# Kernel optimization log

Hardware: AMD Instinct MI355X
Metric: run time of the kernel (lower is better)

Reference implementation:

```python
import jax, jax.numpy as jnp
import numpy as np

TOP_K = 2  # config.num_active_experts


def setup_inputs() -> dict:
    key = jax.random.key(0)
    k1, k2, k3, k4 = jax.random.split(key, 4)
    B, S, D = 2, 2048, 1024
    E, W = 8, 1024  # 8 experts, each width 1024 -> total_expert_width = 8192
    x = jax.random.normal(k1, (B, S, D), dtype=jnp.float32)
    router_w = jax.random.normal(k2, (E, D), dtype=jnp.float32) * 0.02
    w1 = jax.random.normal(k3, (D, E * W), dtype=jnp.float32) * 0.02
    w2 = jax.random.normal(k4, (E * W, D), dtype=jnp.float32) * 0.02
    return {"x": x, "router_w": router_w, "w1": w1, "w2": w2}


def reference(x, router_w, w1, w2):
    B, S, D = x.shape
    E = router_w.shape[0]
    W = w1.shape[1] // E  # uniform expert width
    T = B * S
    xf = x.reshape(T, D)

    # Router: sigmoid gating, top-k, sum-normalized weights (norm_topk_prob)
    router_logits = jnp.einsum('td,ed->te', xf, router_w)
    router_probs = jax.nn.sigmoid(router_logits.astype(jnp.float32))
    top_w, sel = jax.lax.top_k(router_probs, TOP_K)          # [T,K]
    top_w = top_w / (top_w.sum(axis=-1, keepdims=True) + 1e-20)
    top_w = top_w.astype(x.dtype)

    # Expert MLPs: expert e uses w1[:, off_e:off_e+W], w2[off_e:off_e+W, :].
    # Uniform width -> single batched einsum over experts (same math as the
    # padded-gather / block-sparse SDD/DSD grouped GEMM pipeline).
    W1e = w1.reshape(D, E, W).transpose(1, 0, 2)             # [E,D,W]
    W2e = w2.reshape(E, W, D)                                # [E,W,D]
    h = jnp.einsum('td,edw->etw', xf, W1e)                   # up-proj
    a = jnp.square(jax.nn.relu(h))                           # relu_squared
    y = jnp.einsum('etw,ewd->etd', a, W2e)                   # down-proj

    # Weighted scatter-combine: combine_weights[t,e] = top_w if e selected else 0
    cw = jnp.zeros((T, E), dtype=x.dtype).at[jnp.arange(T)[:, None], sel].set(top_w)
    out = jnp.einsum('etd,te->td', y, cw)
    return out.reshape(B, S, D)
```

## Files before the change

### kernel.cpp

```cpp
#include <hip/hip_runtime.h>
#include <hip/hip_bf16.h>


#define T_TOKENS 4096
#define DD 1024
#define EE 8
#define WW 1024
#define CAP 1536
#define BM 128
#define BN 128
#define BK 64
#define MT (CAP / BM)
#define NT (WW / BN)
#define GEMM_BLOCKS (EE * MT * NT)
#define TR1_BLOCKS 2048
#define TR2_BLOCKS 2048

typedef short bf16x8 __attribute__((ext_vector_type(8)));
typedef float f32x4 __attribute__((ext_vector_type(4)));

__device__ __forceinline__ void gload_lds16(const void* g, void* l) {
  __builtin_amdgcn_global_load_lds((__attribute__((address_space(1))) void*)(g),
                                   (__attribute__((address_space(3))) void*)(l),
                                   16, 0, 0);
}

__device__ __forceinline__ float bf2f(unsigned short u) {
  union { unsigned int i; float f; } v; v.i = (unsigned int)u << 16; return v.f;
}

__global__ __launch_bounds__(256) void pre_kernel(
    const float* __restrict__ w1, const float* __restrict__ x,
    const float* __restrict__ rw,
    __hip_bfloat16* __restrict__ w1t, __hip_bfloat16* __restrict__ xb,
    int* __restrict__ sel, float* __restrict__ wpair)
{
  __shared__ float tile[64][65];
  int b = blockIdx.x;
  if (b < TR1_BLOCKS) {
    int bx = b & 15;
    int by = b >> 4;
    const float* src = w1;
    __hip_bfloat16* dst = w1t;
    long src_ld = EE * WW, dst_ld = DD;
    long c0 = (long)bx * 64;
    long r0 = (long)by * 64;
    int tx = threadIdx.x & 15, ty = threadIdx.x >> 4;
#pragma unroll
    for (int i = 0; i < 4; i++) {
      int sr = ty + 16 * i;
      f32x4 v = *(const f32x4*)(src + (c0 + sr) * src_ld + r0 + tx * 4);
      tile[sr][tx * 4 + 0] = v[0];
      tile[sr][tx * 4 + 1] = v[1];
      tile[sr][tx * 4 + 2] = v[2];
      tile[sr][tx * 4 + 3] = v[3];
    }
    __syncthreads();
#pragma unroll
    for (int i = 0; i < 4; i++) {
      int dr = ty + 16 * i;
      union { __hip_bfloat16 hb[4]; ushort4 u4; } pk;
#pragma unroll
      for (int j = 0; j < 4; j++)
        pk.hb[j] = __float2bfloat16(tile[tx * 4 + j][dr]);
      *(ushort4*)((unsigned short*)dst + (r0 + dr) * dst_ld + c0 + tx * 4) = pk.u4;
    }
  } else {
    int lane = threadIdx.x & 63;
    int wave = threadIdx.x >> 6;
    int t = (b - TR1_BLOCKS) * 4 + wave;
    const float* xrow = x + (size_t)t * DD;
    float acc[EE];
#pragma unroll
    for (int e = 0; e < EE; e++) acc[e] = 0.f;
#pragma unroll
    for (int i = 0; i < DD / 64; i++) {
      int d = lane + i * 64;
      float xv = xrow[d];
      xb[t * DD + d] = __float2bfloat16(xv);
#pragma unroll
      for (int e = 0; e < EE; e++) acc[e] += xv * rw[e * DD + d];
    }
#pragma unroll
    for (int e = 0; e < EE; e++) {
#pragma unroll
      for (int off = 32; off > 0; off >>= 1)
        acc[e] += __shfl_down(acc[e], off, 64);
    }
    if (lane == 0) {
      float p[EE];
#pragma unroll
      for (int e = 0; e < EE; e++) p[e] = 1.f / (1.f + expf(-acc[e]));
      int e0 = 0; float b0 = p[0];
      for (int e = 1; e < EE; e++) if (p[e] > b0) { b0 = p[e]; e0 = e; }
      int e1 = -1; float b1 = -1.f;
      for (int e = 0; e < EE; e++) {
        if (e == e0) continue;
        if (p[e] > b1) { b1 = p[e]; e1 = e; }
      }
      float s = b0 + b1 + 1e-20f;
      sel[t] = e0 | (e1 << 8);
      wpair[2 * t]     = b0 / s;
      wpair[2 * t + 1] = b1 / s;
    }
  }
}

__global__ __launch_bounds__(1024) void build_lists(
    const int* __restrict__ sel, int* __restrict__ counts,
    int* __restrict__ idx, int* __restrict__ tslot)
{
  __shared__ int lcnt[EE];
  int tid = threadIdx.x, lane = tid & 63;
  if (tid < EE) lcnt[tid] = 0;
  __syncthreads();
  unsigned long long lower = (1ull << lane) - 1;
#pragma unroll
  for (int j = 0; j < T_TOKENS / 1024; j++) {
    int t = j * 1024 + tid;
    int s = sel[t];
    int e0 = s & 0xff, e1 = (s >> 8) & 0xff;
    int slot0 = 0, slot1 = 0;
#pragma unroll
    for (int e = 0; e < EE; e++) {
      unsigned long long m0 = __ballot(e0 == e);
      unsigned long long m1 = __ballot(e1 == e);
      int c0 = __popcll(m0), c1 = __popcll(m1);
      int base = 0;
      if (lane == 0 && (c0 + c1) > 0) base = atomicAdd(&lcnt[e], c0 + c1);
      base = __shfl(base, 0, 64);
      if (e0 == e) slot0 = base + __popcll(m0 & lower);
      if (e1 == e) slot1 = base + c0 + __popcll(m1 & lower);
    }
    int p0 = e0 * CAP + slot0, p1 = e1 * CAP + slot1;
    idx[p0] = t; idx[p1] = t;
    tslot[2 * t] = p0; tslot[2 * t + 1] = p1;
  }
  __syncthreads();
  if (tid < EE) counts[tid] = lcnt[tid];
}

__global__ __launch_bounds__(256, 3) void gemm1_kernel(
    const __hip_bfloat16* __restrict__ xb, const __hip_bfloat16* __restrict__ w1t,
    const int* __restrict__ counts, const int* __restrict__ idx,
    __hip_bfloat16* __restrict__ act,
    const float* __restrict__ w2, __hip_bfloat16* __restrict__ w2t)
{
  __shared__ __attribute__((aligned(16))) char smem[32768];
  int bid = blockIdx.x;
  if (bid >= GEMM_BLOCKS) {
    float (*tile)[65] = (float (*)[65])smem;
    int b2 = bid - GEMM_BLOCKS;
    int bx = b2 & 15;
    int z = b2 >> 4;
    int e = z >> 4, yy = z & 15;
    const float* src = w2 + (long)e * WW * DD;
    __hip_bfloat16* dst = w2t + (long)e * DD * WW;
    long src_ld = DD, dst_ld = WW;
    long c0 = (long)bx * 64;
    long r0 = (long)yy * 64;
    int tx = threadIdx.x & 15, ty = threadIdx.x >> 4;
#pragma unroll
    for (int i = 0; i < 4; i++) {
      int sr = ty + 16 * i;
      f32x4 v = *(const f32x4*)(src + (c0 + sr) * src_ld + r0 + tx * 4);
      tile[sr][tx * 4 + 0] = v[0];
      tile[sr][tx * 4 + 1] = v[1];
      tile[sr][tx * 4 + 2] = v[2];
      tile[sr][tx * 4 + 3] = v[3];
    }
    __syncthreads();
#pragma unroll
    for (int i = 0; i < 4; i++) {
      int dr = ty + 16 * i;
      union { __hip_bfloat16 hb[4]; ushort4 u4; } pk;
#pragma unroll
      for (int j = 0; j < 4; j++)
        pk.hb[j] = __float2bfloat16(tile[tx * 4 + j][dr]);
      *(ushort4*)((unsigned short*)dst + (r0 + dr) * dst_ld + c0 + tx * 4) = pk.u4;
    }
    return;
  }
  short* As = (short*)smem;
  short* Bs = (short*)(smem + 16384);
  int e = bid & 7;
  int i = bid >> 3;
  int mt = i >> 3, nt = i & 7;
  int n_e = counts[e];
  if (mt * BM >= n_e) return;

  int tid = threadIdx.x;
  int lane = tid & 63;
  int wave = __builtin_amdgcn_readfirstlane(tid >> 6);
  int wm = (wave >> 1) * 64, wn = (wave & 1) * 64;
  int m16 = lane & 15, qd = lane >> 4;

  const __hip_bfloat16* gA[4];
  const __hip_bfloat16* gB[4];
#pragma unroll
  for (int i2 = 0; i2 < 4; i2++) {
    int s = i2 * 256 + tid;
    int r = s >> 3;
    int q = (s & 7) ^ (r & 7);
    int rowA = mt * BM + r;
    int slot = rowA < n_e ? rowA : n_e - 1;
    int tok = idx[e * CAP + slot];
    gA[i2] = xb + (size_t)tok * DD + q * 8;
    gB[i2] = w1t + ((size_t)e * WW + nt * BN + r) * DD + q * 8;
  }
  short* ldsA[4];
  short* ldsB[4];
#pragma unroll
  for (int i2 = 0; i2 < 4; i2++) {
    ldsA[i2] = As + (i2 * 256 + wave * 64) * 8;
    ldsB[i2] = Bs + (i2 * 256 + wave * 64) * 8;
  }

  int aoff[4][2], boff[4][2];
#pragma unroll
  for (int mi = 0; mi < 4; mi++) {
    int r = wm + mi * 16 + m16;
#pragma unroll
    for (int h = 0; h < 2; h++)
      aoff[mi][h] = (r * 8 + ((qd + h * 4) ^ (r & 7))) * 8;
  }
#pragma unroll
  for (int ni = 0; ni < 4; ni++) {
    int r = wn + ni * 16 + m16;
#pragma unroll
    for (int h = 0; h < 2; h++)
      boff[ni][h] = (r * 8 + ((qd + h * 4) ^ (r & 7))) * 8;
  }

  f32x4 zero = {0.f, 0.f, 0.f, 0.f};
  f32x4 acc[4][4];
#pragma unroll
  for (int mi = 0; mi < 4; mi++)
#pragma unroll
    for (int ni = 0; ni < 4; ni++) acc[mi][ni] = zero;

  for (int k0 = 0; k0 < DD; k0 += BK) {
#pragma unroll
    for (int i2 = 0; i2 < 4; i2++) gload_lds16(gA[i2] + k0, ldsA[i2]);
#pragma unroll
    for (int i2 = 0; i2 < 4; i2++) gload_lds16(gB[i2] + k0, ldsB[i2]);
    __syncthreads();
#pragma unroll
    for (int h = 0; h < 2; h++) {
      bf16x8 af[4], bfr[4];
#pragma unroll
      for (int mi = 0; mi < 4; mi++) af[mi] = *(const bf16x8*)(As + aoff[mi][h]);
#pragma unroll
      for (int ni = 0; ni < 4; ni++) bfr[ni] = *(const bf16x8*)(Bs + boff[ni][h]);
#pragma unroll
      for (int mi = 0; mi < 4; mi++)
#pragma unroll
        for (int ni = 0; ni < 4; ni++)
          acc[mi][ni] = __builtin_amdgcn_mfma_f32_16x16x32_bf16(
              af[mi], bfr[ni], acc[mi][ni], 0, 0, 0);
    }
    __syncthreads();
  }

#pragma unroll
  for (int mi = 0; mi < 4; mi++) {
#pragma unroll
    for (int reg = 0; reg < 4; reg++) {
      int rowt = mt * BM + wm + mi * 16 + qd * 4 + reg;
      if (rowt < n_e) {
#pragma unroll
        for (int ni = 0; ni < 4; ni++) {
          float v = acc[mi][ni][reg];
          v = v > 0.f ? v * v : 0.f;
          int col = nt * BN + wn + ni * 16 + m16;
          act[((size_t)e * CAP + rowt) * WW + col] = __float2bfloat16(v);
        }
      }
    }
  }
}

__global__ __launch_bounds__(256, 3) void gemm2_kernel(
    const __hip_bfloat16* __restrict__ act, const __hip_bfloat16* __restrict__ w2t,
    const int* __restrict__ counts, __hip_bfloat16* __restrict__ y)
{
  __shared__ __attribute__((aligned(16))) char smem[32768];
  short* As = (short*)smem;
  short* Bs = (short*)(smem + 16384);
  int bid = blockIdx.x;
  int e = bid & 7;
  int i = bid >> 3;
  int mt = i >> 3, nt = i & 7;
  int n_e = counts[e];
  if (mt * BM >= n_e) return;

  int tid = threadIdx.x;
  int lane = tid & 63;
  int wave = __builtin_amdgcn_readfirstlane(tid >> 6);
  int wm = (wave >> 1) * 64, wn = (wave & 1) * 64;
  int m16 = lane & 15, qd = lane >> 4;

  const __hip_bfloat16* gA[4];
  const __hip_bfloat16* gB[4];
#pragma unroll
  for (int i2 = 0; i2 < 4; i2++) {
    int s = i2 * 256 + tid;
    int r = s >> 3;
    int q = (s & 7) ^ (r & 7);
    gA[i2] = act + ((size_t)e * CAP + mt * BM + r) * WW + q * 8;
    gB[i2] = w2t + ((size_t)e * DD + nt * BN + r) * WW + q * 8;
  }
  short* ldsA[4];
  short* ldsB[4];
#pragma unroll
  for (int i2 = 0; i2 < 4; i2++) {
    ldsA[i2] = As + (i2 * 256 + wave * 64) * 8;
    ldsB[i2] = Bs + (i2 * 256 + wave * 64) * 8;
  }

  int aoff[4][2], boff[4][2];
#pragma unroll
  for (int mi = 0; mi < 4; mi++) {
    int r = wm + mi * 16 + m16;
#pragma unroll
    for (int h = 0; h < 2; h++)
      aoff[mi][h] = (r * 8 + ((qd + h * 4) ^ (r & 7))) * 8;
  }
#pragma unroll
  for (int ni = 0; ni < 4; ni++) {
    int r = wn + ni * 16 + m16;
#pragma unroll
    for (int h = 0; h < 2; h++)
      boff[ni][h] = (r * 8 + ((qd + h * 4) ^ (r & 7))) * 8;
  }

  f32x4 zero = {0.f, 0.f, 0.f, 0.f};
  f32x4 acc[4][4];
#pragma unroll
  for (int mi = 0; mi < 4; mi++)
#pragma unroll
    for (int ni = 0; ni < 4; ni++) acc[mi][ni] = zero;

  for (int k0 = 0; k0 < WW; k0 += BK) {
#pragma unroll
    for (int i2 = 0; i2 < 4; i2++) gload_lds16(gA[i2] + k0, ldsA[i2]);
#pragma unroll
    for (int i2 = 0; i2 < 4; i2++) gload_lds16(gB[i2] + k0, ldsB[i2]);
    __syncthreads();
#pragma unroll
    for (int h = 0; h < 2; h++) {
      bf16x8 af[4], bfr[4];
#pragma unroll
      for (int mi = 0; mi < 4; mi++) af[mi] = *(const bf16x8*)(As + aoff[mi][h]);
#pragma unroll
      for (int ni = 0; ni < 4; ni++) bfr[ni] = *(const bf16x8*)(Bs + boff[ni][h]);
#pragma unroll
      for (int mi = 0; mi < 4; mi++)
#pragma unroll
        for (int ni = 0; ni < 4; ni++)
          acc[mi][ni] = __builtin_amdgcn_mfma_f32_16x16x32_bf16(
              af[mi], bfr[ni], acc[mi][ni], 0, 0, 0);
    }
    __syncthreads();
  }

#pragma unroll
  for (int mi = 0; mi < 4; mi++) {
#pragma unroll
    for (int reg = 0; reg < 4; reg++) {
      int slot = mt * BM + wm + mi * 16 + qd * 4 + reg;
      if (slot < n_e) {
#pragma unroll
        for (int ni = 0; ni < 4; ni++) {
          int col = nt * BN + wn + ni * 16 + m16;
          y[((size_t)e * CAP + slot) * DD + col] = __float2bfloat16(acc[mi][ni][reg]);
        }
      }
    }
  }
}

__global__ __launch_bounds__(256) void combine_kernel(
    const __hip_bfloat16* __restrict__ y, const int* __restrict__ tslot,
    const float* __restrict__ wpair, float* __restrict__ out)
{
  int t = blockIdx.x;
  int c = threadIdx.x * 4;
  int s0 = tslot[2 * t], s1 = tslot[2 * t + 1];
  float w0 = wpair[2 * t], w1 = wpair[2 * t + 1];
  const unsigned short* yu = (const unsigned short*)y;
  ushort4 a = *(const ushort4*)(yu + (size_t)s0 * DD + c);
  ushort4 bq = *(const ushort4*)(yu + (size_t)s1 * DD + c);
  f32x4 o;
  o[0] = w0 * bf2f(a.x) + w1 * bf2f(bq.x);
  o[1] = w0 * bf2f(a.y) + w1 * bf2f(bq.y);
  o[2] = w0 * bf2f(a.z) + w1 * bf2f(bq.z);
  o[3] = w0 * bf2f(a.w) + w1 * bf2f(bq.w);
  *(f32x4*)(out + (size_t)t * DD + c) = o;
}

extern "C" void kernel_launch(void* const* d_in, const int* in_sizes, int n_in,
                              void* d_out, int out_size, void* d_ws, size_t ws_size,
                              hipStream_t stream)
{
  const float* x  = (const float*)d_in[0];
  const float* rw = (const float*)d_in[1];
  const float* w1 = (const float*)d_in[2];
  const float* w2 = (const float*)d_in[3];
  float* out = (float*)d_out;

  char* ws = (char*)d_ws;
  __hip_bfloat16* xb  = (__hip_bfloat16*)ws;  ws += (size_t)T_TOKENS * DD * 2;
  __hip_bfloat16* w1t = (__hip_bfloat16*)ws;  ws += (size_t)EE * WW * DD * 2;
  __hip_bfloat16* w2t = (__hip_bfloat16*)ws;  ws += (size_t)EE * DD * WW * 2;
  __hip_bfloat16* act = (__hip_bfloat16*)ws;  ws += (size_t)EE * CAP * WW * 2;
  __hip_bfloat16* y   = (__hip_bfloat16*)ws;  ws += (size_t)EE * CAP * DD * 2;
  int*   counts = (int*)ws;                   ws += 256;
  int*   idx    = (int*)ws;                   ws += (size_t)EE * CAP * 4;
  int*   sel    = (int*)ws;                   ws += (size_t)T_TOKENS * 4;
  int*   tslot  = (int*)ws;                   ws += (size_t)T_TOKENS * 8;
  float* wpair  = (float*)ws;                 ws += (size_t)T_TOKENS * 8;

  pre_kernel<<<TR1_BLOCKS + T_TOKENS / 4, 256, 0, stream>>>(
      w1, x, rw, w1t, xb, sel, wpair);
  build_lists<<<1, 1024, 0, stream>>>(sel, counts, idx, tslot);
  gemm1_kernel<<<GEMM_BLOCKS + TR2_BLOCKS, 256, 0, stream>>>(
      xb, w1t, counts, idx, act, w2, w2t);
  gemm2_kernel<<<GEMM_BLOCKS, 256, 0, stream>>>(act, w2t, counts, y);
  combine_kernel<<<T_TOKENS, 256, 0, stream>>>(y, tslot, wpair, out);
}
```

Measured before the change: 189.5 us.

## Double-buffer LDS in both expert GEMMs and move w2 transpose into list-building kernel

Both grouped GEMMs now keep two LDS stages, so the next K-tile's global-to-LDS loads are issued before the MFMAs on the current tile. This hides load latency and leaves one barrier per iteration instead of two. LDS use doubles to 64KB per block and launch bounds drop to 2 blocks per CU, trading occupancy for overlap. The w2 fp32-to-bf16 transpose moves out of gemm1 into the single-block build_lists launch, which grows to 513 blocks of 1024 threads. That keeps the tail blocks out of gemm1 and runs the transpose alongside list building.

```diff
diff --git a/kernel.cpp b/kernel.cpp
--- a/kernel.cpp
+++ b/kernel.cpp
@@ -14,7 +14,6 @@
 #define NT (WW / BN)
 #define GEMM_BLOCKS (EE * MT * NT)
 #define TR1_BLOCKS 2048
-#define TR2_BLOCKS 2048
 
 typedef short bf16x8 __attribute__((ext_vector_type(8)));
 typedef float f32x4 __attribute__((ext_vector_type(4)));
@@ -106,68 +105,62 @@
   }
 }
 
-__global__ __launch_bounds__(1024) void build_lists(
+__global__ __launch_bounds__(1024) void lists_w2t_kernel(
     const int* __restrict__ sel, int* __restrict__ counts,
-    int* __restrict__ idx, int* __restrict__ tslot)
-{
+    int* __restrict__ idx, int* __restrict__ tslot,
+    const float* __restrict__ w2, __hip_bfloat16* __restrict__ w2t)
+{
+  __shared__ float tile[4][64][65];
   __shared__ int lcnt[EE];
-  int tid = threadIdx.x, lane = tid & 63;
-  if (tid < EE) lcnt[tid] = 0;
-  __syncthreads();
-  unsigned long long lower = (1ull << lane) - 1;
-#pragma unroll
-  for (int j = 0; j < T_TOKENS / 1024; j++) {
-    int t = j * 1024 + tid;
-    int s = sel[t];
-    int e0 = s & 0xff, e1 = (s >> 8) & 0xff;
-    int slot0 = 0, slot1 = 0;
-#pragma unroll
-    for (int e = 0; e < EE; e++) {
-      unsigned long long m0 = __ballot(e0 == e);
-      unsigned long long m1 = __ballot(e1 == e);
-      int c0 = __popcll(m0), c1 = __popcll(m1);
-      int base = 0;
-      if (lane == 0 && (c0 + c1) > 0) base = atomicAdd(&lcnt[e], c0 + c1);
-      base = __shfl(base, 0, 64);
-      if (e0 == e) slot0 = base + __popcll(m0 & lower);
-      if (e1 == e) slot1 = base + c0 + __popcll(m1 & lower);
-    }
-    int p0 = e0 * CAP + slot0, p1 = e1 * CAP + slot1;
-    idx[p0] = t; idx[p1] = t;
-    tslot[2 * t] = p0; tslot[2 * t + 1] = p1;
-  }
-  __syncthreads();
-  if (tid < EE) counts[tid] = lcnt[tid];
-}
-
-__global__ __launch_bounds__(256, 3) void gemm1_kernel(
-    const __hip_bfloat16* __restrict__ xb, const __hip_bfloat16* __restrict__ w1t,
-    const int* __restrict__ counts, const int* __restrict__ idx,
-    __hip_bfloat16* __restrict__ act,
-    const float* __restrict__ w2, __hip_bfloat16* __restrict__ w2t)
-{
-  __shared__ __attribute__((aligned(16))) char smem[32768];
-  int bid = blockIdx.x;
-  if (bid >= GEMM_BLOCKS) {
-    float (*tile)[65] = (float (*)[65])smem;
-    int b2 = bid - GEMM_BLOCKS;
-    int bx = b2 & 15;
-    int z = b2 >> 4;
-    int e = z >> 4, yy = z & 15;
+  int b = blockIdx.x;
+  int tid = threadIdx.x;
+  if (b == 0) {
+    int lane = tid & 63;
+    if (tid < EE) lcnt[tid] = 0;
+    __syncthreads();
+    unsigned long long lower = (1ull << lane) - 1;
+#pragma unroll
+    for (int j = 0; j < T_TOKENS / 1024; j++) {
+      int t = j * 1024 + tid;
+      int s = sel[t];
+      int e0 = s & 0xff, e1 = (s >> 8) & 0xff;
+      int slot0 = 0, slot1 = 0;
+#pragma unroll
+      for (int e = 0; e < EE; e++) {
+        unsigned long long m0 = __ballot(e0 == e);
+        unsigned long long m1 = __ballot(e1 == e);
+        int c0 = __popcll(m0), c1 = __popcll(m1);
+        int base = 0;
+        if (lane == 0 && (c0 + c1) > 0) base = atomicAdd(&lcnt[e], c0 + c1);
+        base = __shfl(base, 0, 64);
+        if (e0 == e) slot0 = base + __popcll(m0 & lower);
+        if (e1 == e) slot1 = base + c0 + __popcll(m1 & lower);
+      }
+      int p0 = e0 * CAP + slot0, p1 = e1 * CAP + slot1;
+      idx[p0] = t; idx[p1] = t;
+      tslot[2 * t] = p0; tslot[2 * t + 1] = p1;
+    }
+    __syncthreads();
+    if (tid < EE) counts[tid] = lcnt[tid];
+  } else {
+    int q = tid >> 8, tq = tid & 255;
+    int z = (b - 1) * 4 + q;
+    int bx = z & 15;
+    int zz = z >> 4;
+    int e = zz >> 4, yy = zz & 15;
     const float* src = w2 + (long)e * WW * DD;
     __hip_bfloat16* dst = w2t + (long)e * DD * WW;
-    long src_ld = DD, dst_ld = WW;
     long c0 = (long)bx * 64;
     long r0 = (long)yy * 64;
-    int tx = threadIdx.x & 15, ty = threadIdx.x >> 4;
+    int tx = tq & 15, ty = tq >> 4;
 #pragma unroll
     for (int i = 0; i < 4; i++) {
       int sr = ty + 16 * i;
-      f32x4 v = *(const f32x4*)(src + (c0 + sr) * src_ld + r0 + tx * 4);
-      tile[sr][tx * 4 + 0] = v[0];
-      tile[sr][tx * 4 + 1] = v[1];
-      tile[sr][tx * 4 + 2] = v[2];
-      tile[sr][tx * 4 + 3] = v[3];
+      f32x4 v = *(const f32x4*)(src + (c0 + sr) * DD + r0 + tx * 4);
+      tile[q][sr][tx * 4 + 0] = v[0];
+      tile[q][sr][tx * 4 + 1] = v[1];
+      tile[q][sr][tx * 4 + 2] = v[2];
+      tile[q][sr][tx * 4 + 3] = v[3];
     }
     __syncthreads();
 #pragma unroll
@@ -176,13 +169,19 @@
       union { __hip_bfloat16 hb[4]; ushort4 u4; } pk;
 #pragma unroll
       for (int j = 0; j < 4; j++)
-        pk.hb[j] = __float2bfloat16(tile[tx * 4 + j][dr]);
-      *(ushort4*)((unsigned short*)dst + (r0 + dr) * dst_ld + c0 + tx * 4) = pk.u4;
-    }
-    return;
-  }
-  short* As = (short*)smem;
-  short* Bs = (short*)(smem + 16384);
+        pk.hb[j] = __float2bfloat16(tile[q][tx * 4 + j][dr]);
+      *(ushort4*)((unsigned short*)dst + (r0 + dr) * WW + c0 + tx * 4) = pk.u4;
+    }
+  }
+}
+
+__global__ __launch_bounds__(256, 2) void gemm1_kernel(
+    const __hip_bfloat16* __restrict__ xb, const __hip_bfloat16* __restrict__ w1t,
+    const int* __restrict__ counts, const int* __restrict__ idx,
+    __hip_bfloat16* __restrict__ act)
+{
+  __shared__ __attribute__((aligned(16))) char smem[65536];
+  int bid = blockIdx.x;
   int e = bid & 7;
   int i = bid >> 3;
   int mt = i >> 3, nt = i & 7;
@@ -208,13 +207,9 @@
     gA[i2] = xb + (size_t)tok * DD + q * 8;
     gB[i2] = w1t + ((size_t)e * WW + nt * BN + r) * DD + q * 8;
   }
-  short* ldsA[4];
-  short* ldsB[4];
-#pragma unroll
-  for (int i2 = 0; i2 < 4; i2++) {
-    ldsA[i2] = As + (i2 * 256 + wave * 64) * 8;
-    ldsB[i2] = Bs + (i2 * 256 + wave * 64) * 8;
-  }
+  int ldsOff[4];
+#pragma unroll
+  for (int i2 = 0; i2 < 4; i2++) ldsOff[i2] = (i2 * 256 + wave * 64) * 8;
 
   int aoff[4][2], boff[4][2];
 #pragma unroll
@@ -239,12 +234,25 @@
 #pragma unroll
     for (int ni = 0; ni < 4; ni++) acc[mi][ni] = zero;
 
+#pragma unroll
+  for (int i2 = 0; i2 < 4; i2++) {
+    gload_lds16(gA[i2], (short*)smem + ldsOff[i2]);
+    gload_lds16(gB[i2], (short*)(smem + 16384) + ldsOff[i2]);
+  }
+  __syncthreads();
+
+  int cur = 0;
   for (int k0 = 0; k0 < DD; k0 += BK) {
-#pragma unroll
-    for (int i2 = 0; i2 < 4; i2++) gload_lds16(gA[i2] + k0, ldsA[i2]);
-#pragma unroll
-    for (int i2 = 0; i2 < 4; i2++) gload_lds16(gB[i2] + k0, ldsB[i2]);
-    __syncthreads();
+    if (k0 + BK < DD) {
+      char* nb = smem + (cur ^ 1) * 32768;
+#pragma unroll
+      for (int i2 = 0; i2 < 4; i2++) {
+        gload_lds16(gA[i2] + k0 + BK, (short*)nb + ldsOff[i2]);
+        gload_lds16(gB[i2] + k0 + BK, (short*)(nb + 16384) + ldsOff[i2]);
+      }
+    }
+    short* As = (short*)(smem + cur * 32768);
+    short* Bs = (short*)(smem + cur * 32768 + 16384);
 #pragma unroll
     for (int h = 0; h < 2; h++) {
       bf16x8 af[4], bfr[4];
@@ -260,6 +268,7 @@
               af[mi], bfr[ni], acc[mi][ni], 0, 0, 0);
     }
     __syncthreads();
+    cur ^= 1;
   }
 
 #pragma unroll
@@ -280,13 +289,11 @@
   }
 }
 
-__global__ __launch_bounds__(256, 3) void gemm2_kernel(
+__global__ __launch_bounds__(256, 2) void gemm2_kernel(
     const __hip_bfloat16* __restrict__ act, const __hip_bfloat16* __restrict__ w2t,
     const int* __restrict__ counts, __hip_bfloat16* __restrict__ y)
 {
-  __shared__ __attribute__((aligned(16))) char smem[32768];
-  short* As = (short*)smem;
-  short* Bs = (short*)(smem + 16384);
+  __shared__ __attribute__((aligned(16))) char smem[65536];
   int bid = blockIdx.x;
   int e = bid & 7;
   int i = bid >> 3;
@@ -310,13 +317,9 @@
     gA[i2] = act + ((size_t)e * CAP + mt * BM + r) * WW + q * 8;
     gB[i2] = w2t + ((size_t)e * DD + nt * BN + r) * WW + q * 8;
   }
-  short* ldsA[4];
-  short* ldsB[4];
-#pragma unroll
-  for (int i2 = 0; i2 < 4; i2++) {
-    ldsA[i2] = As + (i2 * 256 + wave * 64) * 8;
-    ldsB[i2] = Bs + (i2 * 256 + wave * 64) * 8;
-  }
+  int ldsOff[4];
+#pragma unroll
+  for (int i2 = 0; i2 < 4; i2++) ldsOff[i2] = (i2 * 256 + wave * 64) * 8;
 
   int aoff[4][2], boff[4][2];
 #pragma unroll
@@ -341,12 +344,25 @@
 #pragma unroll
     for (int ni = 0; ni < 4; ni++) acc[mi][ni] = zero;
 
+#pragma unroll
+  for (int i2 = 0; i2 < 4; i2++) {
+    gload_lds16(gA[i2], (short*)smem + ldsOff[i2]);
+    gload_lds16(gB[i2], (short*)(smem + 16384) + ldsOff[i2]);
+  }
+  __syncthreads();
+
+  int cur = 0;
   for (int k0 = 0; k0 < WW; k0 += BK) {
-#pragma unroll
-    for (int i2 = 0; i2 < 4; i2++) gload_lds16(gA[i2] + k0, ldsA[i2]);
-#pragma unroll
-    for (int i2 = 0; i2 < 4; i2++) gload_lds16(gB[i2] + k0, ldsB[i2]);
-    __syncthreads();
+    if (k0 + BK < WW) {
+      char* nb = smem + (cur ^ 1) * 32768;
+#pragma unroll
+      for (int i2 = 0; i2 < 4; i2++) {
+        gload_lds16(gA[i2] + k0 + BK, (short*)nb + ldsOff[i2]);
+        gload_lds16(gB[i2] + k0 + BK, (short*)(nb + 16384) + ldsOff[i2]);
+      }
+    }
+    short* As = (short*)(smem + cur * 32768);
+    short* Bs = (short*)(smem + cur * 32768 + 16384);
 #pragma unroll
     for (int h = 0; h < 2; h++) {
       bf16x8 af[4], bfr[4];
@@ -362,6 +378,7 @@
               af[mi], bfr[ni], acc[mi][ni], 0, 0, 0);
     }
     __syncthreads();
+    cur ^= 1;
   }
 
 #pragma unroll
@@ -423,9 +440,8 @@
 
   pre_kernel<<<TR1_BLOCKS + T_TOKENS / 4, 256, 0, stream>>>(
       w1, x, rw, w1t, xb, sel, wpair);
-  build_lists<<<1, 1024, 0, stream>>>(sel, counts, idx, tslot);
-  gemm1_kernel<<<GEMM_BLOCKS + TR2_BLOCKS, 256, 0, stream>>>(
-      xb, w1t, counts, idx, act, w2, w2t);
+  lists_w2t_kernel<<<513, 1024, 0, stream>>>(sel, counts, idx, tslot, w2, w2t);
+  gemm1_kernel<<<GEMM_BLOCKS, 256, 0, stream>>>(xb, w1t, counts, idx, act);
   gemm2_kernel<<<GEMM_BLOCKS, 256, 0, stream>>>(act, w2t, counts, y);
   combine_kernel<<<T_TOKENS, 256, 0, stream>>>(y, tslot, wpair, out);
 }
```

Result: slower. 195.5 us (+3.2%).
